# Optimization experiments

Measured on AMD Instinct MI355X. Metric: run time of the kernel, lower is better.

## Reference

```python
import jax, jax.numpy as jnp
import numpy as np

EMBED_DIM = 1024
NUM_HEADS = 16
HEAD_DIM = EMBED_DIM // NUM_HEADS
RANK = 512
B, S = 4, 4096


def setup_inputs() -> dict:
    key = jax.random.key(0)
    ks = jax.random.split(key, 16)
    sd = 0.02
    inp = {
        "query": jax.random.normal(ks[0], (B, S, EMBED_DIM), jnp.float32),
        "key": jax.random.normal(ks[1], (B, S, EMBED_DIM), jnp.float32),
        "value": jax.random.normal(ks[2], (B, S, EMBED_DIM), jnp.float32),
        # torch nn.Linear weights: [out_features, in_features]
        "q_down_w": jax.random.normal(ks[3], (RANK, EMBED_DIM), jnp.float32) * sd,
        "q_up_w": jax.random.normal(ks[4], (EMBED_DIM, RANK), jnp.float32) * sd,
        "q_up_b": jax.random.normal(ks[5], (EMBED_DIM,), jnp.float32) * sd,
        "k_down_w": jax.random.normal(ks[6], (RANK, EMBED_DIM), jnp.float32) * sd,
        "k_up_w": jax.random.normal(ks[7], (EMBED_DIM, RANK), jnp.float32) * sd,
        "k_up_b": jax.random.normal(ks[8], (EMBED_DIM,), jnp.float32) * sd,
        "v_down_w": jax.random.normal(ks[9], (RANK, EMBED_DIM), jnp.float32) * sd,
        "v_up_w": jax.random.normal(ks[10], (EMBED_DIM, RANK), jnp.float32) * sd,
        "v_up_b": jax.random.normal(ks[11], (EMBED_DIM,), jnp.float32) * sd,
        "out_w": jax.random.normal(ks[12], (EMBED_DIM, EMBED_DIM), jnp.float32) * sd,
        "out_b": jax.random.normal(ks[13], (EMBED_DIM,), jnp.float32) * sd,
    }
    return inp


def _linear(x, w, b=None):
    y = x @ w.T
    return y if b is None else y + b


def reference(query, key, value,
              q_down_w, q_up_w, q_up_b,
              k_down_w, k_up_w, k_up_b,
              v_down_w, v_up_w, v_up_b,
              out_w, out_b):
    b, s, _ = query.shape
    # low-rank QKV projections
    q = _linear(_linear(query, q_down_w), q_up_w, q_up_b)
    k = _linear(_linear(key, k_down_w), k_up_w, k_up_b)
    v = _linear(_linear(value, v_down_w), v_up_w, v_up_b)
    # [B,S,E] -> [B,H,S,Dh]
    q = q.reshape(b, s, NUM_HEADS, HEAD_DIM).transpose(0, 2, 1, 3)
    k = k.reshape(b, s, NUM_HEADS, HEAD_DIM).transpose(0, 2, 1, 3)
    v = v.reshape(b, s, NUM_HEADS, HEAD_DIM).transpose(0, 2, 1, 3)
    # kernel feature map: elu + 1  (note: scaling_factor in original is computed but unused)
    q = jax.nn.elu(q) + 1.0
    k = jax.nn.elu(k) + 1.0
    k_sum = k.sum(axis=-2)                              # [B,H,Dh]
    denom = jnp.einsum('bhnd,bhd->bhn', q, k_sum)       # [B,H,S]
    kv = jnp.einsum('bhnd,bhne->bhde', k, v)            # [B,H,Dh,Dh]
    num = jnp.einsum('bhnd,bhde->bhne', q, kv)          # [B,H,S,Dh]
    out = num / (denom[..., None] + 1e-6)
    out = out.transpose(0, 2, 1, 3).reshape(b, s, EMBED_DIM)
    return _linear(out, out_w, out_b)
```

## Files before the change

kernel.cpp:

```cpp
#include <hip/hip_runtime.h>
#include <hip/hip_bf16.h>

typedef unsigned short ushort_t;
typedef unsigned int uint_t;
typedef __attribute__((ext_vector_type(8))) short short8;
typedef __attribute__((ext_vector_type(4))) float f32x4;

#define EMBED 1024
#define RANK  512
#define BB    4
#define SS    4096
#define HH    16
#define DHD   64
#define MM    (BB*SS)
#define NCHUNK 16

__device__ __forceinline__ float bf2f(ushort_t u) {
    union { uint_t i; float f; } v; v.i = ((uint_t)u) << 16; return v.f;
}
__device__ __forceinline__ ushort_t f2bf(float f) {
    union { float f; uint_t i; } v; v.f = f;
    uint_t r = v.i + 0x7FFFu + ((v.i >> 16) & 1u);
    return (ushort_t)(r >> 16);
}
__device__ __forceinline__ void gl2lds16(const void* g, void* l) {
    __builtin_amdgcn_global_load_lds((const __attribute__((address_space(1))) void*)g,
                                     (__attribute__((address_space(3))) void*)l,
                                     16, 0, 0);
}

template<int EPI>
__global__ __launch_bounds__(256) void gemm_bt(
    const ushort_t* __restrict__ A0, const ushort_t* __restrict__ A1, const ushort_t* __restrict__ A2,
    const ushort_t* __restrict__ B0, const ushort_t* __restrict__ B1, const ushort_t* __restrict__ B2,
    const float* __restrict__ bias0, const float* __restrict__ bias1, const float* __restrict__ bias2,
    void* __restrict__ C0, void* __restrict__ C1, void* __restrict__ C2,
    int N, int K, int nbx)
{
    __shared__ __align__(16) char lds_raw[49152];

    const int z = blockIdx.z;
    const ushort_t* Ab   = (z == 0) ? A0 : (z == 1) ? A1 : A2;
    const ushort_t* Bm   = (z == 0) ? B0 : (z == 1) ? B1 : B2;
    const float*    bias = (z == 0) ? bias0 : (z == 1) ? bias1 : bias2;
    void*           Cv   = (z == 0) ? C0 : (z == 1) ? C1 : C2;

    const int cpx = gridDim.x >> 3;
    const int bid = blockIdx.x;
    const int wg  = (bid & 7) * cpx + (bid >> 3);
    const long m0 = (long)(wg / nbx) * 128;
    const long n0 = (long)(wg % nbx) * 128;

    const int t = threadIdx.x;
    const int lane = t & 63;
    const int w = t >> 6;
    const int wr = (w >> 1) * 64;
    const int wc = (w & 1) * 64;
    const int fr = lane & 15;
    const int kq = (lane >> 4) * 8;

    const int srow = t >> 2;
    const int scol = ((t & 3) ^ ((srow >> 1) & 3)) * 8;
    const int kqs = (((kq >> 3) ^ ((fr >> 1) & 3))) * 8;

    auto STAGE = [&](int k0, int buf) {
        char* Ad = lds_raw + buf * 8192;
        char* Bd = lds_raw + 24576 + buf * 8192;
        #pragma unroll
        for (int ro = 0; ro < 2; ++ro) {
            const int row = ro * 64 + srow;
            gl2lds16(Ab + (m0 + row) * (long)K + k0 + scol, Ad + (ro * 256 + w * 64) * 16);
            gl2lds16(Bm + (n0 + row) * (long)K + k0 + scol, Bd + (ro * 256 + w * 64) * 16);
        }
    };

    f32x4 acc[4][4] = {};
    const int nt = K >> 5;

    STAGE(0, 0);
    STAGE(32, 1);

    int cur = 0;
    for (int ti = 0; ti < nt; ++ti) {
        if (ti + 1 < nt) { asm volatile("s_waitcnt vmcnt(4)" ::: "memory"); }
        else             { asm volatile("s_waitcnt vmcnt(0)" ::: "memory"); }
        __builtin_amdgcn_sched_barrier(0);
        __builtin_amdgcn_s_barrier();
        __builtin_amdgcn_sched_barrier(0);

        int nb = cur + 2; if (nb >= 3) nb -= 3;
        if (ti + 2 < nt) STAGE((ti + 2) << 5, nb);

        const ushort_t* Asc = (const ushort_t*)(lds_raw + cur * 8192);
        const ushort_t* Bsc = (const ushort_t*)(lds_raw + 24576 + cur * 8192);
        short8 av[4], bv[4];
        #pragma unroll
        for (int mi = 0; mi < 4; ++mi)
            av[mi] = *(const short8*)&Asc[(wr + mi * 16 + fr) * 32 + kqs];
        #pragma unroll
        for (int nf = 0; nf < 4; ++nf)
            bv[nf] = *(const short8*)&Bsc[(wc + nf * 16 + fr) * 32 + kqs];
        #pragma unroll
        for (int mi = 0; mi < 4; ++mi)
            #pragma unroll
            for (int nf = 0; nf < 4; ++nf)
                acc[mi][nf] = __builtin_amdgcn_mfma_f32_16x16x32_bf16(
                    av[mi], bv[nf], acc[mi][nf], 0, 0, 0);

        ++cur; if (cur == 3) cur = 0;
    }

    const int rj = (lane >> 4) * 4;
    if (EPI == 3) {
        float* Cf = (float*)Cv;
        __syncthreads();
        #pragma unroll
        for (int nf = 0; nf < 4; ++nf) {
            const long col = n0 + wc + nf * 16 + fr;
            const float bval = bias[col];
            #pragma unroll
            for (int mi = 0; mi < 4; ++mi)
                #pragma unroll
                for (int j = 0; j < 4; ++j)
                    Cf[(m0 + wr + mi * 16 + rj + j) * (long)N + col] = acc[mi][nf][j] + bval;
        }
    } else {
        ushort_t* Ct = (ushort_t*)lds_raw;
        __syncthreads();
        const bool do_elu = (EPI == 2) && (z < 2);
        #pragma unroll
        for (int nf = 0; nf < 4; ++nf) {
            const int coll = wc + nf * 16 + fr;
            const float bval = (EPI >= 2) ? bias[n0 + coll] : 0.0f;
            #pragma unroll
            for (int mi = 0; mi < 4; ++mi) {
                #pragma unroll
                for (int j = 0; j < 4; ++j) {
                    float x = acc[mi][nf][j];
                    if (EPI >= 2) x += bval;
                    if (do_elu) x = (x > 0.0f) ? (x + 1.0f) : __expf(x);
                    Ct[(wr + mi * 16 + rj + j) * 128 + coll] = f2bf(x);
                }
            }
        }
        __syncthreads();
        ushort_t* Cb = (ushort_t*)Cv;
        #pragma unroll
        for (int it = 0; it < 8; ++it) {
            const int idx = it * 256 + t;
            const int r   = idx >> 4;
            const int c8  = (idx & 15) * 8;
            short8 vv = *(const short8*)&Ct[r * 128 + c8];
            *(short8*)(Cb + (m0 + r) * (long)N + n0 + c8) = vv;
        }
    }
}

__global__ __launch_bounds__(256) void cvt_act(const float* __restrict__ q,
                                               const float* __restrict__ k,
                                               const float* __restrict__ v,
                                               ushort_t* __restrict__ qo,
                                               ushort_t* __restrict__ ko,
                                               ushort_t* __restrict__ vo)
{
    const int zz = blockIdx.y;
    const float* src = (zz == 0) ? q : (zz == 1) ? k : v;
    ushort_t*    dst = (zz == 0) ? qo : (zz == 1) ? ko : vo;
    const long i = ((long)blockIdx.x * 256 + threadIdx.x) * 8;
    f32x4 f0 = *(const f32x4*)(src + i);
    f32x4 f1 = *(const f32x4*)(src + i + 4);
    short8 h;
    h[0] = (short)f2bf(f0[0]); h[1] = (short)f2bf(f0[1]);
    h[2] = (short)f2bf(f0[2]); h[3] = (short)f2bf(f0[3]);
    h[4] = (short)f2bf(f1[0]); h[5] = (short)f2bf(f1[1]);
    h[6] = (short)f2bf(f1[2]); h[7] = (short)f2bf(f1[3]);
    *(short8*)(dst + i) = h;
}

__global__ __launch_bounds__(256) void cvt_weights(
    const float* __restrict__ s0, const float* __restrict__ s1,
    const float* __restrict__ s2, const float* __restrict__ s3,
    const float* __restrict__ s4, const float* __restrict__ s5,
    const float* __restrict__ s6,
    ushort_t* __restrict__ d0, ushort_t* __restrict__ d1,
    ushort_t* __restrict__ d2, ushort_t* __restrict__ d3,
    ushort_t* __restrict__ d4, ushort_t* __restrict__ d5,
    ushort_t* __restrict__ d6)
{
    const int y = blockIdx.y;
    const float* src; ushort_t* dst; int n;
    switch (y) {
        case 0: src = s0; dst = d0; n = RANK * EMBED; break;
        case 1: src = s1; dst = d1; n = RANK * EMBED; break;
        case 2: src = s2; dst = d2; n = RANK * EMBED; break;
        case 3: src = s3; dst = d3; n = RANK * EMBED; break;
        case 4: src = s4; dst = d4; n = RANK * EMBED; break;
        case 5: src = s5; dst = d5; n = RANK * EMBED; break;
        default: src = s6; dst = d6; n = EMBED * EMBED; break;
    }
    const int i = (blockIdx.x * 256 + threadIdx.x) * 4;
    if (i < n) {
        f32x4 f = *(const f32x4*)(src + i);
        typedef __attribute__((ext_vector_type(4))) short short4v;
        short4v h;
        h[0] = (short)f2bf(f[0]); h[1] = (short)f2bf(f[1]);
        h[2] = (short)f2bf(f[2]); h[3] = (short)f2bf(f[3]);
        *(short4v*)(dst + i) = h;
    }
}

__global__ __launch_bounds__(256) void kv_stats(const ushort_t* __restrict__ Kp,
                                                const ushort_t* __restrict__ Vp,
                                                float* __restrict__ kvp,
                                                float* __restrict__ ksump)
{
    __shared__ __align__(16) ushort_t Ks[64 * 64];
    __shared__ __align__(16) ushort_t Vs[64 * 64];
    const int t = threadIdx.x;
    const int w = t >> 6;
    const int bh = blockIdx.x;
    const int chunk = blockIdx.y;
    const int b = bh >> 4, h = bh & 15;
    const int d0 = (t & 15) * 4;
    const int e0 = (t >> 4) * 4;
    float acc[4][4] = {};
    float sks[4] = {};
    const long hbase = ((long)b * SS) * EMBED + h * DHD;

    for (int sub = 0; sub < 4; ++sub) {
        const int n00 = chunk * 256 + sub * 64;
        #pragma unroll
        for (int ro = 0; ro < 2; ++ro) {
            const int idx = ro * 256 + t;
            const int r = idx >> 3, c16 = idx & 7;
            const long g = hbase + (long)(n00 + r) * EMBED + c16 * 8;
            gl2lds16(Kp + g, (char*)Ks + (ro * 256 + w * 64) * 16);
            gl2lds16(Vp + g, (char*)Vs + (ro * 256 + w * 64) * 16);
        }
        __syncthreads();
        #pragma unroll 8
        for (int n = 0; n < 64; ++n) {
            const uint_t* kr = (const uint_t*)(Ks + n * 64 + d0);
            const uint_t* vr = (const uint_t*)(Vs + n * 64 + e0);
            const uint_t k01 = kr[0], k23 = kr[1];
            const uint_t v01 = vr[0], v23 = vr[1];
            float kd[4], ve[4];
            {
                union { uint_t i; float f; } a, bq, c, dq;
                a.i = k01 << 16; bq.i = k01 & 0xffff0000u;
                c.i = k23 << 16; dq.i = k23 & 0xffff0000u;
                kd[0] = a.f; kd[1] = bq.f; kd[2] = c.f; kd[3] = dq.f;
            }
            {
                union { uint_t i; float f; } a, bq, c, dq;
                a.i = v01 << 16; bq.i = v01 & 0xffff0000u;
                c.i = v23 << 16; dq.i = v23 & 0xffff0000u;
                ve[0] = a.f; ve[1] = bq.f; ve[2] = c.f; ve[3] = dq.f;
            }
            #pragma unroll
            for (int e = 0; e < 4; ++e)
                #pragma unroll
                for (int d = 0; d < 4; ++d)
                    acc[e][d] += ve[e] * kd[d];
            if (e0 == 0) {
                #pragma unroll
                for (int d = 0; d < 4; ++d) sks[d] += kd[d];
            }
        }
        __syncthreads();
    }

    float* dst = kvp + ((long)chunk * 64 + bh) * 4096;
    #pragma unroll
    for (int e = 0; e < 4; ++e) {
        f32x4 vv; vv[0] = acc[e][0]; vv[1] = acc[e][1]; vv[2] = acc[e][2]; vv[3] = acc[e][3];
        *(f32x4*)(dst + (e0 + e) * 64 + d0) = vv;
    }
    if (e0 == 0) {
        float* sd = ksump + ((long)chunk * 64 + bh) * 64 + d0;
        #pragma unroll
        for (int d = 0; d < 4; ++d) sd[d] = sks[d];
    }
}

__global__ __launch_bounds__(256) void kv_reduce(const float* __restrict__ kvp,
                                                 const float* __restrict__ ksump,
                                                 ushort_t* __restrict__ kvb,
                                                 float* __restrict__ ksumf)
{
    const int bh = blockIdx.x;
    const int t = threadIdx.x;
    const long base = (long)bh * 4096 + t * 16;
    f32x4 s[4] = {};
    #pragma unroll 4
    for (int c = 0; c < NCHUNK; ++c) {
        const float* src = kvp + (long)c * 64 * 4096 + base;
        #pragma unroll
        for (int j = 0; j < 4; ++j) s[j] += *(const f32x4*)(src + j * 4);
    }
    short8 o0, o1;
    #pragma unroll
    for (int j = 0; j < 4; ++j) {
        o0[j]     = (short)f2bf(s[0][j]); o0[4 + j] = (short)f2bf(s[1][j]);
        o1[j]     = (short)f2bf(s[2][j]); o1[4 + j] = (short)f2bf(s[3][j]);
    }
    *(short8*)(kvb + base)     = o0;
    *(short8*)(kvb + base + 8) = o1;

    if (t < 64) {
        float ss = 0.f;
        #pragma unroll
        for (int c = 0; c < NCHUNK; ++c) ss += ksump[(long)c * 64 * 64 + bh * 64 + t];
        ksumf[bh * 64 + t] = ss;
    }
}

__global__ __launch_bounds__(256) void attn_out(const ushort_t* __restrict__ Qp,
                                                const ushort_t* __restrict__ kvb,
                                                const float* __restrict__ ksum,
                                                ushort_t* __restrict__ Op)
{
    __shared__ __align__(16) ushort_t Qs[128 * 64];
    __shared__ __align__(16) ushort_t KVs[64 * 64];
    __shared__ float kss[64];
    __shared__ float dnm[128];
    const int t = threadIdx.x;
    const int w = t >> 6, lane = t & 63;
    const int bh = blockIdx.x, mc = blockIdx.y;
    const int b = bh >> 4, h = bh & 15;
    const long base = ((long)b * SS + mc * 128) * EMBED + h * DHD;

    #pragma unroll
    for (int ro = 0; ro < 4; ++ro) {
        const int idx = ro * 256 + t;
        const int r = idx >> 3, c16 = idx & 7;
        gl2lds16(Qp + base + (long)r * EMBED + c16 * 8,
                 (char*)Qs + (ro * 256 + w * 64) * 16);
    }
    #pragma unroll
    for (int ro = 0; ro < 2; ++ro) {
        const int idx = ro * 256 + t;
        gl2lds16(kvb + (long)bh * 4096 + idx * 8,
                 (char*)KVs + (ro * 256 + w * 64) * 16);
    }
    if (t < 64) kss[t] = ksum[bh * 64 + t];
    __syncthreads();

    if (t < 128) {
        float s = 0.f;
        const uint_t* qr = (const uint_t*)(Qs + t * 64);
        #pragma unroll
        for (int jj = 0; jj < 32; ++jj) {
            const uint_t u = qr[jj];
            union { uint_t i; float f; } lo, hi;
            lo.i = u << 16; hi.i = u & 0xffff0000u;
            s += lo.f * kss[2 * jj] + hi.f * kss[2 * jj + 1];
        }
        dnm[t] = s;
    }

    const int fr = lane & 15, kq = (lane >> 4) * 8;
    f32x4 acc[2][4] = {};
    #pragma unroll
    for (int ks = 0; ks < 2; ++ks) {
        short8 av[2], bv[4];
        #pragma unroll
        for (int mi = 0; mi < 2; ++mi)
            av[mi] = *(const short8*)&Qs[(w * 32 + mi * 16 + fr) * 64 + ks * 32 + kq];
        #pragma unroll
        for (int nf = 0; nf < 4; ++nf)
            bv[nf] = *(const short8*)&KVs[(nf * 16 + fr) * 64 + ks * 32 + kq];
        #pragma unroll
        for (int mi = 0; mi < 2; ++mi)
            #pragma unroll
            for (int nf = 0; nf < 4; ++nf)
                acc[mi][nf] = __builtin_amdgcn_mfma_f32_16x16x32_bf16(
                    av[mi], bv[nf], acc[mi][nf], 0, 0, 0);
    }
    __syncthreads();

    const int rj = (lane >> 4) * 4;
    #pragma unroll
    for (int mi = 0; mi < 2; ++mi) {
        #pragma unroll
        for (int nf = 0; nf < 4; ++nf) {
            #pragma unroll
            for (int j = 0; j < 4; ++j) {
                const int r = w * 32 + mi * 16 + rj + j;
                const int c = nf * 16 + fr;
                const float x = acc[mi][nf][j] / (dnm[r] + 1e-6f);
                Op[base + (long)r * EMBED + c] = f2bf(x);
            }
        }
    }
}

extern "C" void kernel_launch(void* const* d_in, const int* in_sizes, int n_in,
                              void* d_out, int out_size, void* d_ws, size_t ws_size,
                              hipStream_t stream)
{
    (void)in_sizes; (void)n_in; (void)out_size; (void)ws_size;
    const float* query = (const float*)d_in[0];
    const float* key_  = (const float*)d_in[1];
    const float* value = (const float*)d_in[2];
    const float* q_dw  = (const float*)d_in[3];
    const float* q_uw  = (const float*)d_in[4];
    const float* q_ub  = (const float*)d_in[5];
    const float* k_dw  = (const float*)d_in[6];
    const float* k_uw  = (const float*)d_in[7];
    const float* k_ub  = (const float*)d_in[8];
    const float* v_dw  = (const float*)d_in[9];
    const float* v_uw  = (const float*)d_in[10];
    const float* v_ub  = (const float*)d_in[11];
    const float* o_w   = (const float*)d_in[12];
    const float* o_b   = (const float*)d_in[13];

    char* ws = (char*)d_ws;
    size_t off = 0;
    auto alloc = [&](size_t bytes) -> void* {
        void* p = ws + off;
        off += (bytes + 255) & ~(size_t)255;
        return p;
    };
    const size_t WSMALL = (size_t)RANK * EMBED;
    ushort_t* bw_qd = (ushort_t*)alloc(WSMALL * 2);
    ushort_t* bw_qu = (ushort_t*)alloc(WSMALL * 2);
    ushort_t* bw_kd = (ushort_t*)alloc(WSMALL * 2);
    ushort_t* bw_ku = (ushort_t*)alloc(WSMALL * 2);
    ushort_t* bw_vd = (ushort_t*)alloc(WSMALL * 2);
    ushort_t* bw_vu = (ushort_t*)alloc(WSMALL * 2);
    ushort_t* bw_o  = (ushort_t*)alloc((size_t)EMBED * EMBED * 2);
    ushort_t* Qb    = (ushort_t*)alloc((size_t)MM * EMBED * 2);
    ushort_t* Kb    = (ushort_t*)alloc((size_t)MM * EMBED * 2);
    ushort_t* Vb    = (ushort_t*)alloc((size_t)MM * EMBED * 2);
    ushort_t* Y1q   = (ushort_t*)alloc((size_t)MM * RANK * 2);
    ushort_t* Y1k   = (ushort_t*)alloc((size_t)MM * RANK * 2);
    ushort_t* Y1v   = (ushort_t*)alloc((size_t)MM * RANK * 2);
    float*    ksump = (float*)alloc((size_t)NCHUNK * 64 * 64 * 4);
    float*    ksumf = (float*)alloc((size_t)64 * 64 * 4);
    ushort_t* kvb   = (ushort_t*)alloc((size_t)64 * 64 * 64 * 2);

    ushort_t* PQ = Qb;
    ushort_t* PK = Kb;
    ushort_t* PV = Vb;
    float*    kvp = (float*)Y1q;
    ushort_t* O   = Y1k;

    const dim3 blk(256);

    cvt_act<<<dim3((size_t)MM * EMBED / 2048, 3), blk, 0, stream>>>(
        query, key_, value, Qb, Kb, Vb);
    cvt_weights<<<dim3(EMBED * EMBED / 1024, 7), blk, 0, stream>>>(
        q_dw, q_uw, k_dw, k_uw, v_dw, v_uw, o_w,
        bw_qd, bw_qu, bw_kd, bw_ku, bw_vd, bw_vu, bw_o);

    gemm_bt<0><<<dim3(MM / 128 * (RANK / 128), 1, 3), blk, 0, stream>>>(
        Qb, Kb, Vb,
        bw_qd, bw_kd, bw_vd,
        nullptr, nullptr, nullptr,
        Y1q, Y1k, Y1v,
        RANK, EMBED, RANK / 128);

    gemm_bt<2><<<dim3(MM / 128 * (EMBED / 128), 1, 3), blk, 0, stream>>>(
        Y1q, Y1k, Y1v,
        bw_qu, bw_ku, bw_vu,
        q_ub, k_ub, v_ub,
        PQ, PK, PV,
        EMBED, RANK, EMBED / 128);

    kv_stats<<<dim3(64, NCHUNK), blk, 0, stream>>>(PK, PV, kvp, ksump);
    kv_reduce<<<dim3(64), blk, 0, stream>>>(kvp, ksump, kvb, ksumf);
    attn_out<<<dim3(64, 32), blk, 0, stream>>>(PQ, kvb, ksumf, O);

    gemm_bt<3><<<dim3(MM / 128 * (EMBED / 128), 1, 1), blk, 0, stream>>>(
        O, nullptr, nullptr,
        bw_o, nullptr, nullptr,
        o_b, nullptr, nullptr,
        d_out, nullptr, nullptr,
        EMBED, EMBED, EMBED / 128);
}
```

Measured before the change: 299.8 us.

## Fuse fp32-to-bf16 activation conversion into down-projection GEMM A-tile loads

Removes the separate cvt_act pass that turned the fp32 query/key/value into bf16 copies. A new gemm_dn kernel reads the fp32 activations straight into registers, converts them to bf16, and writes them into swizzled LDS while the B tile is staged asynchronously, all double-buffered. This avoids a full write plus re-read of three bf16 activation tensors. The cost is that the GEMM now reads fp32 A tiles (twice the bytes) and does conversion work inside its loop. The epilogue LDS row stride also changes from 128 to 136 to reduce bank conflicts.

```diff
diff --git a/kernel.cpp b/kernel.cpp
--- a/kernel.cpp
+++ b/kernel.cpp
@@ -139,7 +139,7 @@
                     float x = acc[mi][nf][j];
                     if (EPI >= 2) x += bval;
                     if (do_elu) x = (x > 0.0f) ? (x + 1.0f) : __expf(x);
-                    Ct[(wr + mi * 16 + rj + j) * 128 + coll] = f2bf(x);
+                    Ct[(wr + mi * 16 + rj + j) * 136 + coll] = f2bf(x);
                 }
             }
         }
@@ -150,31 +150,134 @@
             const int idx = it * 256 + t;
             const int r   = idx >> 4;
             const int c8  = (idx & 15) * 8;
-            short8 vv = *(const short8*)&Ct[r * 128 + c8];
+            short8 vv = *(const short8*)&Ct[r * 136 + c8];
             *(short8*)(Cb + (m0 + r) * (long)N + n0 + c8) = vv;
         }
     }
 }
 
-__global__ __launch_bounds__(256) void cvt_act(const float* __restrict__ q,
-                                               const float* __restrict__ k,
-                                               const float* __restrict__ v,
-                                               ushort_t* __restrict__ qo,
-                                               ushort_t* __restrict__ ko,
-                                               ushort_t* __restrict__ vo)
-{
-    const int zz = blockIdx.y;
-    const float* src = (zz == 0) ? q : (zz == 1) ? k : v;
-    ushort_t*    dst = (zz == 0) ? qo : (zz == 1) ? ko : vo;
-    const long i = ((long)blockIdx.x * 256 + threadIdx.x) * 8;
-    f32x4 f0 = *(const f32x4*)(src + i);
-    f32x4 f1 = *(const f32x4*)(src + i + 4);
-    short8 h;
-    h[0] = (short)f2bf(f0[0]); h[1] = (short)f2bf(f0[1]);
-    h[2] = (short)f2bf(f0[2]); h[3] = (short)f2bf(f0[3]);
-    h[4] = (short)f2bf(f1[0]); h[5] = (short)f2bf(f1[1]);
-    h[6] = (short)f2bf(f1[2]); h[7] = (short)f2bf(f1[3]);
-    *(short8*)(dst + i) = h;
+__global__ __launch_bounds__(256) void gemm_dn(
+    const float* __restrict__ A0, const float* __restrict__ A1, const float* __restrict__ A2,
+    const ushort_t* __restrict__ B0, const ushort_t* __restrict__ B1, const ushort_t* __restrict__ B2,
+    void* __restrict__ C0, void* __restrict__ C1, void* __restrict__ C2,
+    int N, int K, int nbx)
+{
+    __shared__ __align__(16) char lds_raw[36864];
+
+    const int z = blockIdx.z;
+    const float*    Af = (z == 0) ? A0 : (z == 1) ? A1 : A2;
+    const ushort_t* Bm = (z == 0) ? B0 : (z == 1) ? B1 : B2;
+    void*           Cv = (z == 0) ? C0 : (z == 1) ? C1 : C2;
+
+    const int cpx = gridDim.x >> 3;
+    const int bid = blockIdx.x;
+    const int wg  = (bid & 7) * cpx + (bid >> 3);
+    const long m0 = (long)(wg / nbx) * 128;
+    const long n0 = (long)(wg % nbx) * 128;
+
+    const int t = threadIdx.x;
+    const int lane = t & 63;
+    const int w = t >> 6;
+    const int wr = (w >> 1) * 64;
+    const int wc = (w & 1) * 64;
+    const int fr = lane & 15;
+    const int kq = (lane >> 4) * 8;
+
+    const int srow = t >> 2;
+    const int scol = ((t & 3) ^ ((srow >> 1) & 3)) * 8;
+    const int kqs = (((kq >> 3) ^ ((fr >> 1) & 3))) * 8;
+
+    const int arow  = t >> 1;
+    const int acolh = (t & 1) * 16;
+    const int asw   = (arow >> 1) & 3;
+    const int as0   = (2 * (t & 1)) ^ asw;
+    const int as1   = (2 * (t & 1) + 1) ^ asw;
+
+    auto LOADA = [&](int k0, f32x4* ra) {
+        const float* src = Af + (m0 + arow) * (long)K + k0 + acolh;
+        #pragma unroll
+        for (int j = 0; j < 4; ++j) ra[j] = *(const f32x4*)(src + 4 * j);
+    };
+    auto LOADB = [&](int k0, int buf) {
+        char* Bd = lds_raw + 16384 + buf * 8192;
+        #pragma unroll
+        for (int ro = 0; ro < 2; ++ro) {
+            const int row = ro * 64 + srow;
+            gl2lds16(Bm + (n0 + row) * (long)K + k0 + scol, Bd + (ro * 256 + w * 64) * 16);
+        }
+    };
+    auto WRITEA = [&](const f32x4* ra, int buf) {
+        ushort_t* Ad = (ushort_t*)(lds_raw + buf * 8192);
+        short8 h0, h1;
+        #pragma unroll
+        for (int j = 0; j < 4; ++j) {
+            h0[2 * j]     = (short)f2bf(ra[j >> 1][(j & 1) * 2]);
+            h0[2 * j + 1] = (short)f2bf(ra[j >> 1][(j & 1) * 2 + 1]);
+            h1[2 * j]     = (short)f2bf(ra[2 + (j >> 1)][(j & 1) * 2]);
+            h1[2 * j + 1] = (short)f2bf(ra[2 + (j >> 1)][(j & 1) * 2 + 1]);
+        }
+        *(short8*)&Ad[arow * 32 + as0 * 8] = h0;
+        *(short8*)&Ad[arow * 32 + as1 * 8] = h1;
+    };
+
+    f32x4 acc[4][4] = {};
+    const int nt = K >> 5;
+
+    f32x4 ra[4];
+    LOADA(0, ra);
+    LOADB(0, 0);
+    WRITEA(ra, 0);
+    __syncthreads();
+
+    int cur = 0;
+    for (int ti = 0; ti < nt; ++ti) {
+        if (ti + 1 < nt) {
+            LOADA((ti + 1) << 5, ra);
+            LOADB((ti + 1) << 5, cur ^ 1);
+        }
+
+        const ushort_t* Asc = (const ushort_t*)(lds_raw + cur * 8192);
+        const ushort_t* Bsc = (const ushort_t*)(lds_raw + 16384 + cur * 8192);
+        short8 av[4], bv[4];
+        #pragma unroll
+        for (int mi = 0; mi < 4; ++mi)
+            av[mi] = *(const short8*)&Asc[(wr + mi * 16 + fr) * 32 + kqs];
+        #pragma unroll
+        for (int nf = 0; nf < 4; ++nf)
+            bv[nf] = *(const short8*)&Bsc[(wc + nf * 16 + fr) * 32 + kqs];
+        #pragma unroll
+        for (int mi = 0; mi < 4; ++mi)
+            #pragma unroll
+            for (int nf = 0; nf < 4; ++nf)
+                acc[mi][nf] = __builtin_amdgcn_mfma_f32_16x16x32_bf16(
+                    av[mi], bv[nf], acc[mi][nf], 0, 0, 0);
+
+        if (ti + 1 < nt) WRITEA(ra, cur ^ 1);
+        __syncthreads();
+        cur ^= 1;
+    }
+
+    ushort_t* Ct = (ushort_t*)lds_raw;
+    const int rj = (lane >> 4) * 4;
+    #pragma unroll
+    for (int nf = 0; nf < 4; ++nf) {
+        const int coll = wc + nf * 16 + fr;
+        #pragma unroll
+        for (int mi = 0; mi < 4; ++mi)
+            #pragma unroll
+            for (int j = 0; j < 4; ++j)
+                Ct[(wr + mi * 16 + rj + j) * 136 + coll] = f2bf(acc[mi][nf][j]);
+    }
+    __syncthreads();
+    ushort_t* Cb = (ushort_t*)Cv;
+    #pragma unroll
+    for (int it = 0; it < 8; ++it) {
+        const int idx = it * 256 + t;
+        const int r   = idx >> 4;
+        const int c8  = (idx & 15) * 8;
+        short8 vv = *(const short8*)&Ct[r * 136 + c8];
+        *(short8*)(Cb + (m0 + r) * (long)N + n0 + c8) = vv;
+    }
 }
 
 __global__ __launch_bounds__(256) void cvt_weights(
@@ -430,9 +533,9 @@
     ushort_t* bw_vd = (ushort_t*)alloc(WSMALL * 2);
     ushort_t* bw_vu = (ushort_t*)alloc(WSMALL * 2);
     ushort_t* bw_o  = (ushort_t*)alloc((size_t)EMBED * EMBED * 2);
-    ushort_t* Qb    = (ushort_t*)alloc((size_t)MM * EMBED * 2);
-    ushort_t* Kb    = (ushort_t*)alloc((size_t)MM * EMBED * 2);
-    ushort_t* Vb    = (ushort_t*)alloc((size_t)MM * EMBED * 2);
+    ushort_t* PQ    = (ushort_t*)alloc((size_t)MM * EMBED * 2);
+    ushort_t* PK    = (ushort_t*)alloc((size_t)MM * EMBED * 2);
+    ushort_t* PV    = (ushort_t*)alloc((size_t)MM * EMBED * 2);
     ushort_t* Y1q   = (ushort_t*)alloc((size_t)MM * RANK * 2);
     ushort_t* Y1k   = (ushort_t*)alloc((size_t)MM * RANK * 2);
     ushort_t* Y1v   = (ushort_t*)alloc((size_t)MM * RANK * 2);
@@ -440,24 +543,18 @@
     float*    ksumf = (float*)alloc((size_t)64 * 64 * 4);
     ushort_t* kvb   = (ushort_t*)alloc((size_t)64 * 64 * 64 * 2);
 
-    ushort_t* PQ = Qb;
-    ushort_t* PK = Kb;
-    ushort_t* PV = Vb;
     float*    kvp = (float*)Y1q;
     ushort_t* O   = Y1k;
 
     const dim3 blk(256);
 
-    cvt_act<<<dim3((size_t)MM * EMBED / 2048, 3), blk, 0, stream>>>(
-        query, key_, value, Qb, Kb, Vb);
     cvt_weights<<<dim3(EMBED * EMBED / 1024, 7), blk, 0, stream>>>(
         q_dw, q_uw, k_dw, k_uw, v_dw, v_uw, o_w,
         bw_qd, bw_qu, bw_kd, bw_ku, bw_vd, bw_vu, bw_o);
 
-    gemm_bt<0><<<dim3(MM / 128 * (RANK / 128), 1, 3), blk, 0, stream>>>(
-        Qb, Kb, Vb,
+    gemm_dn<<<dim3(MM / 128 * (RANK / 128), 1, 3), blk, 0, stream>>>(
+        query, key_, value,
         bw_qd, bw_kd, bw_vd,
-        nullptr, nullptr, nullptr,
         Y1q, Y1k, Y1v,
         RANK, EMBED, RANK / 128);
 
```

Result: slower. 318.5 us (+6.2%).
